# Performance work log

Measured on AMD Instinct MI355X. Metric: run time of the kernel, lower is better.

## Reference

```python
import jax, jax.numpy as jnp
import numpy as np

D_MODEL = 512
D_K = 64
D_V = 128
H = D_MODEL // D_V  # 4 heads (num_head = d_model // d_v per the source)
B, N = 4, 2048


def setup_inputs() -> dict:
    key = jax.random.key(0)
    k0, k1, k2, k3, k4 = jax.random.split(key, 5)
    s = 0.02
    return {
        "input_x": jax.random.normal(k0, (B, N, D_MODEL), jnp.float32),
        "Wq": jax.random.normal(k1, (D_MODEL, H * D_K), jnp.float32) * s,
        "Wk": jax.random.normal(k2, (D_MODEL, H * D_K), jnp.float32) * s,
        "Wv": jax.random.normal(k3, (D_MODEL, D_MODEL), jnp.float32) * s,
        "Wo": jax.random.normal(k4, (D_MODEL, D_MODEL), jnp.float32) * s,
    }


def reference(input_x, Wq, Wk, Wv, Wo):
    b, n, _ = input_x.shape
    # Contiguous per-head slices in the source == a simple reshape here.
    q = (input_x @ Wq).reshape(b, n, H, D_K)   # [B,N,H,dk]
    k = (input_x @ Wk).reshape(b, n, H, D_K)   # [B,N,H,dk]
    v = (input_x @ Wv).reshape(b, n, H, D_V)   # [B,N,H,dv]
    scale = jnp.sqrt(jnp.float32(D_K))
    scores = jnp.einsum('bqhd,bkhd->bhqk', q, k) / scale  # [B,H,N,N]
    # FAITHFUL quirk: the source uses nn.Softmax() with no dim on a 3D
    # (B,N,N) tensor; PyTorch's legacy dim inference picks dim=0 (batch).
    attn = jax.nn.softmax(scores, axis=0)
    out = jnp.einsum('bhqk,bkhd->bqhd', attn, v).reshape(b, n, H * D_V)
    return out @ Wo
```

## Files before the change

### kernel.cpp

```cpp
#include <hip/hip_runtime.h>
#include <hip/hip_bf16.h>


typedef __attribute__((ext_vector_type(8))) short short8;
typedef __attribute__((ext_vector_type(4))) float floatx4;
typedef unsigned short u16;
typedef unsigned int u32;

#define MFMA16(a, b, c) __builtin_amdgcn_mfma_f32_16x16x32_bf16((a), (b), (c), 0, 0, 0)

__device__ __forceinline__ u16 f2bf(float f) {
    union { float f; unsigned u; } v; v.f = f;
    unsigned r = v.u + 0x7fffu + ((v.u >> 16) & 1u);
    return (u16)(r >> 16);
}

__device__ __forceinline__ float bf2f(u16 b) {
    union { unsigned u; float f; } v; v.u = ((u32)b) << 16;
    return v.f;
}

__device__ __forceinline__ u32 pk2bf(float a, float b) {
#if __has_builtin(__builtin_amdgcn_cvt_pk_bf16_f32)
    typedef __attribute__((ext_vector_type(2))) __bf16 bf16x2;
    union { bf16x2 v; u32 u; } c;
    c.v = __builtin_amdgcn_cvt_pk_bf16_f32(a, b);
    return c.u;
#else
    return (u32)f2bf(a) | ((u32)f2bf(b) << 16);
#endif
}

__device__ __forceinline__ float ex2(float x) {
#if __has_builtin(__builtin_amdgcn_exp2f)
    return __builtin_amdgcn_exp2f(x);
#else
    return exp2f(x);
#endif
}

__device__ __forceinline__ void gload_lds16(const u16* g, u16* l) {
    __builtin_amdgcn_global_load_lds(
        (const __attribute__((address_space(1))) void*)(const void*)g,
        (__attribute__((address_space(3))) void*)(void*)l, 16, 0, 0);
}

__global__ __launch_bounds__(256) void prep_all_kernel(
    const float* __restrict__ x, u16* __restrict__ xb,
    const float* __restrict__ Wq, const float* __restrict__ Wk,
    const float* __restrict__ Wv, const float* __restrict__ Wo,
    u16* __restrict__ WallT, u16* __restrict__ WoT) {
    int bid = blockIdx.x;
    if (bid < 4096) {
        int i = bid * 256 + threadIdx.x;
        float4 v = ((const float4*)x)[i];
        ushort4 o;
        o.x = f2bf(v.x); o.y = f2bf(v.y); o.z = f2bf(v.z); o.w = f2bf(v.w);
        ((ushort4*)xb)[i] = o;
        return;
    }
    int i = (bid - 4096) * 256 + threadIdx.x;
    if (i < 524288) {
        int n = i >> 9, k = i & 511;
        float v;
        if (n < 256)      v = Wq[k * 256 + n] * 0.18033688011f;
        else if (n < 512) v = Wk[k * 256 + (n - 256)];
        else              v = Wv[k * 512 + (n - 512)];
        WallT[i] = f2bf(v);
    } else {
        int j = i - 524288;
        int n = j >> 9, k = j & 511;
        WoT[j] = f2bf(Wo[k * 512 + n]);
    }
}

__global__ __launch_bounds__(512) void gemm_qkv_kernel(
    const u16* __restrict__ A, const u16* __restrict__ BT,
    u16* __restrict__ Qp, u16* __restrict__ Kp, u16* __restrict__ Vp,
    int Kdim) {
    __shared__ u16 sm[16896];
    u16* Asl = sm;
    u16* Bsl = sm + 8192;
    const int tid = threadIdx.x;
    const int mbase = blockIdx.y * 128;
    const int nbase = blockIdx.x * 128;
    const int wave = tid >> 6, lane = tid & 63;
    const int wm = wave >> 2, wn = wave & 3;
    const int lq = lane & 15, quad = lane >> 4;

    const u16* gA = A + (size_t)(mbase + wave * 16 + (lane >> 3)) * Kdim + (lane & 7) * 8;
    const u16* gB = BT + (size_t)(nbase + wave * 16 + (lane >> 3)) * Kdim + (lane & 7) * 8;
    u16* lA = &Asl[(wave * 16) * 64];
    u16* lB = &Bsl[(wave * 16) * 64];

    const floatx4 z4 = {0.f, 0.f, 0.f, 0.f};
    floatx4 acc[4][2];
#pragma unroll
    for (int i = 0; i < 4; i++)
#pragma unroll
        for (int j = 0; j < 2; j++) acc[i][j] = z4;

    const int nk = Kdim >> 6;
    for (int kk = 0; kk < nk; kk++) {
        const int kb = kk << 6;
        if (kk) __syncthreads();
#pragma unroll
        for (int i = 0; i < 2; i++) {
            gload_lds16(gA + kb + (size_t)(i * 8) * Kdim, lA + (i * 8) * 64);
            gload_lds16(gB + kb + (size_t)(i * 8) * Kdim, lB + (i * 8) * 64);
        }
        __syncthreads();
#pragma unroll
        for (int ki = 0; ki < 2; ki++) {
            short8 af[4], bf[2];
#pragma unroll
            for (int mi = 0; mi < 4; mi++)
                af[mi] = *(const short8*)&Asl[(wm * 64 + mi * 16 + lq) * 64 + ki * 32 + quad * 8];
#pragma unroll
            for (int ni = 0; ni < 2; ni++)
                bf[ni] = *(const short8*)&Bsl[(wn * 32 + ni * 16 + lq) * 64 + ki * 32 + quad * 8];
#pragma unroll
            for (int mi = 0; mi < 4; mi++)
#pragma unroll
                for (int ni = 0; ni < 2; ni++)
                    acc[mi][ni] = MFMA16(af[mi], bf[ni], acc[mi][ni]);
        }
    }
    __syncthreads();
    const bool vtile = (nbase >= 512);
#pragma unroll
    for (int mi = 0; mi < 4; mi++)
#pragma unroll
        for (int ni = 0; ni < 2; ni++) {
            int cl = wn * 32 + ni * 16 + lq;
#pragma unroll
            for (int r = 0; r < 4; r++) {
                int rl = wm * 64 + mi * 16 + quad * 4 + r;
                if (vtile) sm[cl * 132 + rl] = f2bf(acc[mi][ni][r]);
                else       sm[rl * 132 + cl] = f2bf(acc[mi][ni][r]);
            }
        }
    __syncthreads();
    const int b = mbase >> 11;
    const int keyb = mbase & 2047;
    if (nbase < 256) {
        const int hq = nbase >> 6;
        const int qs_base = keyb >> 4;
#pragma unroll
        for (int t = 0; t < 4; t++) {
            int l = wave * 4 + t;
            int qs2 = l >> 2, h2 = (l >> 1) & 1, ki = l & 1;
            int qd = lane >> 4, lqq = lane & 15;
            short8 v = *(const short8*)&sm[(qs2 * 16 + lqq) * 132 + h2 * 64 + ki * 32 + qd * 8];
            int h = hq + h2;
            size_t base = ((size_t)(((b * 4 + h) * 128 + (qs_base + qs2)) * 2 + ki) * 64 + lane) << 3;
            *(short8*)&Qp[base] = v;
        }
    } else if (nbase < 512) {
        const int hb = (nbase - 256) >> 6;
        const int ktb = keyb >> 6;
#pragma unroll
        for (int t = 0; t < 4; t++) {
            int l = wave * 4 + t;
            int kt2 = l >> 4, hf = (l >> 3) & 1, nj = (l >> 2) & 1;
            int h2 = (l >> 1) & 1, ki = l & 1;
            int quadk = lane >> 4, lqk = lane & 15;
            short8 v = *(const short8*)&sm[(kt2 * 64 + hf * 32 + lqk * 2 + nj) * 132 +
                                           h2 * 64 + ki * 32 + quadk * 8];
            int h = hb + h2;
            size_t base = ((size_t)(((((b * 4 + h) * 32 + (ktb + kt2)) * 2 + hf) * 2 + nj)
                                    * 2 + ki) * 64 + lane) << 3;
            *(short8*)&Kp[base] = v;
        }
    } else {
        const int h = (nbase - 512) >> 7;
        const int ktb = keyb >> 6;
#pragma unroll
        for (int t = 0; t < 4; t++) {
            int l = wave * 4 + t;
            int kt2 = l >> 4, hf = (l >> 3) & 1, niv = (l >> 1) & 3, wv = l & 1;
            int quadv = lane >> 4, lqv = lane & 15;
            short8 v = *(const short8*)&sm[(hf * 64 + niv * 16 + lqv) * 132 +
                                           kt2 * 64 + wv * 32 + quadv * 8];
            size_t base = ((size_t)(((((b * 4 + h) * 32 + (ktb + kt2)) * 2 + hf) * 4 + niv)
                                    * 2 + wv) * 64 + lane) << 3;
            *(short8*)&Vp[base] = v;
        }
    }
}

__global__ __launch_bounds__(512) void gemm_out_kernel(
    const u16* __restrict__ A, const u16* __restrict__ BT,
    float* __restrict__ Cf, int Kdim, int ldc) {
    __shared__ u16 Asl[64 * 64];
    __shared__ u16 Bsl[128 * 64];
    const int tid = threadIdx.x;
    const int mbase = blockIdx.y * 64;
    const int nbase = blockIdx.x * 128;
    const int wave = tid >> 6, lane = tid & 63;
    const int wm = wave >> 2, wn = wave & 3;
    const int lq = lane & 15, quad = lane >> 4;

    const u16* gA = A + (size_t)(mbase + wave * 8 + (lane >> 3)) * Kdim + (lane & 7) * 8;
    const u16* gB = BT + (size_t)(nbase + wave * 16 + (lane >> 3)) * Kdim + (lane & 7) * 8;
    u16* lA = &Asl[(wave * 8) * 64];
    u16* lB = &Bsl[(wave * 16) * 64];

    const floatx4 z4 = {0.f, 0.f, 0.f, 0.f};
    floatx4 acc[2][2];
#pragma unroll
    for (int i = 0; i < 2; i++)
#pragma unroll
        for (int j = 0; j < 2; j++) acc[i][j] = z4;

    const int nk = Kdim >> 6;
    for (int kk = 0; kk < nk; kk++) {
        const int kb = kk << 6;
        if (kk) __syncthreads();
        gload_lds16(gA + kb, lA);
        gload_lds16(gB + kb, lB);
        gload_lds16(gB + kb + (size_t)8 * Kdim, lB + 8 * 64);
        __syncthreads();
#pragma unroll
        for (int ki = 0; ki < 2; ki++) {
            short8 af[2], bf[2];
#pragma unroll
            for (int mi = 0; mi < 2; mi++)
                af[mi] = *(const short8*)&Asl[(wm * 32 + mi * 16 + lq) * 64 + ki * 32 + quad * 8];
#pragma unroll
            for (int ni = 0; ni < 2; ni++)
                bf[ni] = *(const short8*)&Bsl[(wn * 32 + ni * 16 + lq) * 64 + ki * 32 + quad * 8];
#pragma unroll
            for (int mi = 0; mi < 2; mi++)
#pragma unroll
                for (int ni = 0; ni < 2; ni++)
                    acc[mi][ni] = MFMA16(af[mi], bf[ni], acc[mi][ni]);
        }
    }
#pragma unroll
    for (int mi = 0; mi < 2; mi++)
#pragma unroll
        for (int ni = 0; ni < 2; ni++)
#pragma unroll
            for (int r = 0; r < 4; r++)
                Cf[(size_t)(mbase + wm * 32 + mi * 16 + quad * 4 + r) * ldc +
                   (nbase + wn * 32 + ni * 16 + lq)] = acc[mi][ni][r];
}

__global__ __launch_bounds__(512) void attn_kernel(const u16* __restrict__ Qp,
                                                   const u16* __restrict__ Kp,
                                                   const u16* __restrict__ Vp,
                                                   u16* __restrict__ Pp) {
    __shared__ u16 pl[2 * 4 * 4096];
    const int bx = blockIdx.x;
    const int h = bx & 3;
    const int ck = (bx >> 2) & 3;
    const int qt = bx >> 4;
    const int tid = threadIdx.x;
    const int wave = tid >> 6, lane = tid & 63;
    const int mi = wave & 3, half = wave >> 2;
    const int dq = wave;
    const int half_v = dq >> 2, ni_v = dq & 3;
    const int lq = lane & 15, quad = lane >> 4;
    const int qs = qt * 4 + mi;

    short8 aq[4][2];
#pragma unroll
    for (int b = 0; b < 4; b++)
#pragma unroll
        for (int ki = 0; ki < 2; ki++)
            aq[b][ki] = *(const short8*)&Qp[
                ((size_t)((((b * 4 + h) * 128 + qs) * 2 + ki) * 64 + lane) << 3)];

    const floatx4 z4 = {0.f, 0.f, 0.f, 0.f};
    floatx4 oacc[4][4];
#pragma unroll
    for (int b = 0; b < 4; b++)
#pragma unroll
        for (int m2 = 0; m2 < 4; m2++) oacc[b][m2] = z4;

    for (int kt = ck * 8; kt < ck * 8 + 8; kt++) {
        u16* plb = &pl[((kt & 1) * 4 + mi) * 4096];
        u16* plbuf = &pl[(kt & 1) * 4 * 4096];
        floatx4 s[4][2];
#pragma unroll
        for (int b = 0; b < 4; b++) {
            const u16* kb = Kp +
                ((size_t)((((b * 4 + h) * 32 + kt) * 2 + half) * 2) << 10) +
                lane * 8;
#pragma unroll
            for (int nj = 0; nj < 2; nj++) {
                s[b][nj] = z4;
#pragma unroll
                for (int ki = 0; ki < 2; ki++)
                    s[b][nj] = MFMA16(aq[b][ki],
                                      *(const short8*)(kb + (nj * 2 + ki) * 512),
                                      s[b][nj]);
            }
        }
        short8 vf[4][2];
#pragma unroll
        for (int b = 0; b < 4; b++) {
            const u16* vb = Vp +
                ((size_t)(((((b * 4 + h) * 32 + kt) * 2 + half_v) * 4 + ni_v) * 2) << 9) +
                lane * 8;
            vf[b][0] = *(const short8*)vb;
            vf[b][1] = *(const short8*)(vb + 512);
        }
#pragma unroll
        for (int r = 0; r < 4; r++) {
            float e0a = ex2(s[0][0][r]), e0b = ex2(s[0][1][r]);
            float e1a = ex2(s[1][0][r]), e1b = ex2(s[1][1][r]);
            float e2a = ex2(s[2][0][r]), e2b = ex2(s[2][1][r]);
            float e3a = ex2(s[3][0][r]), e3b = ex2(s[3][1][r]);
            float ia = __builtin_amdgcn_rcpf(e0a + e1a + e2a + e3a);
            float ib = __builtin_amdgcn_rcpf(e0b + e1b + e2b + e3b);
            int q = quad * 4 + r;
            int col = (half * 32 + 2 * lq) ^ ((q & 7) * 8);
            *(u32*)&plb[(0 * 16 + q) * 64 + col] = pk2bf(e0a * ia, e0b * ib);
            *(u32*)&plb[(1 * 16 + q) * 64 + col] = pk2bf(e1a * ia, e1b * ib);
            *(u32*)&plb[(2 * 16 + q) * 64 + col] = pk2bf(e2a * ia, e2b * ib);
            *(u32*)&plb[(3 * 16 + q) * 64 + col] = pk2bf(e3a * ia, e3b * ib);
        }
        __syncthreads();
        const int sw = (lq & 7) * 8;
#pragma unroll
        for (int b = 0; b < 4; b++) {
#pragma unroll
            for (int m2 = 0; m2 < 4; m2++) {
                const u16* pm = plbuf + m2 * 4096;
                short8 ap0 = *(const short8*)&pm[(b * 16 + lq) * 64 + ((quad * 8) ^ sw)];
                short8 ap1 = *(const short8*)&pm[(b * 16 + lq) * 64 + ((32 + quad * 8) ^ sw)];
                oacc[b][m2] = MFMA16(ap0, vf[b][0], oacc[b][m2]);
                oacc[b][m2] = MFMA16(ap1, vf[b][1], oacc[b][m2]);
            }
        }
    }
    u16* Pc = Pp + (size_t)ck * (8192 * 512);
#pragma unroll
    for (int b = 0; b < 4; b++)
#pragma unroll
        for (int m2 = 0; m2 < 4; m2++)
#pragma unroll
            for (int r = 0; r < 4; r++)
                Pc[(size_t)(b * 2048 + qt * 64 + m2 * 16 + quad * 4 + r) * 512 +
                   h * 128 + dq * 16 + lq] = f2bf(oacc[b][m2][r]);
}

__global__ __launch_bounds__(256) void reduce4_kernel(u16* __restrict__ P) {
    const size_t S = (size_t)8192 * 512;
    size_t i = ((size_t)blockIdx.x * 256 + threadIdx.x) * 8;
    short8 a = *(short8*)&P[i];
    short8 b = *(short8*)&P[i + S];
    short8 c = *(short8*)&P[i + 2 * S];
    short8 d = *(short8*)&P[i + 3 * S];
    short8 o;
#pragma unroll
    for (int j = 0; j < 8; j++) {
        float s = bf2f((u16)a[j]) + bf2f((u16)b[j]) +
                  bf2f((u16)c[j]) + bf2f((u16)d[j]);
        o[j] = (short)f2bf(s);
    }
    *(short8*)&P[i] = o;
}

extern "C" void kernel_launch(void* const* d_in, const int* in_sizes, int n_in,
                              void* d_out, int out_size, void* d_ws, size_t ws_size,
                              hipStream_t stream) {
    const float* x  = (const float*)d_in[0];
    const float* Wq = (const float*)d_in[1];
    const float* Wk = (const float*)d_in[2];
    const float* Wv = (const float*)d_in[3];
    const float* Wo = (const float*)d_in[4];
    float* out = (float*)d_out;

    char* ws = (char*)d_ws;
    u16* Pp    = (u16*)ws;
    u16* Xb    = (u16*)ws;
    u16* WallT = (u16*)(ws + (size_t)8 * 1024 * 1024);
    char* tail = ws + (size_t)32 * 1024 * 1024;
    u16* WoT   = (u16*)tail; tail += (size_t)512 * 512 * 2;
    u16* Qp    = (u16*)tail; tail += (size_t)8192 * 256 * 2;
    u16* Kp    = (u16*)tail; tail += (size_t)8192 * 256 * 2;
    u16* Vp    = (u16*)tail; tail += (size_t)8192 * 512 * 2;

    prep_all_kernel<<<7168, 256, 0, stream>>>(x, Xb, Wq, Wk, Wv, Wo, WallT, WoT);
    gemm_qkv_kernel<<<dim3(8, 64), 512, 0, stream>>>(Xb, WallT, Qp, Kp, Vp, 512);
    attn_kernel<<<512, 512, 0, stream>>>(Qp, Kp, Vp, Pp);
    reduce4_kernel<<<2048, 256, 0, stream>>>(Pp);
    gemm_out_kernel<<<dim3(4, 128), 512, 0, stream>>>(Pp, WoT, out, 512, 512);
}
```

Baseline: 166.2 us.

## Fuse split-K partial reduction into output GEMM, remap blocks per XCD, add setprio

Drops the separate reduce4 kernel. The output GEMM now sums the four split-K partial buffers while it loads its A tile, so it reads them directly instead of using async global-to-LDS copies for A. Block indices in all three kernels are remapped so that neighbouring tiles land on the same XCD, for better L2 locality. s_setprio is raised around the MFMA sections of the attention kernel. This saves one launch and a write/read round trip of P, at the cost of more A traffic (each A tile is reread by four N-blocks) and synchronous loads in the GEMM.

```diff
diff --git a/kernel.cpp b/kernel.cpp
--- a/kernel.cpp
+++ b/kernel.cpp
@@ -82,8 +82,10 @@
     u16* Asl = sm;
     u16* Bsl = sm + 8192;
     const int tid = threadIdx.x;
-    const int mbase = blockIdx.y * 128;
-    const int nbase = blockIdx.x * 128;
+    const int bid0 = blockIdx.y * 8 + blockIdx.x;
+    const int xcd = bid0 & 7, jj = bid0 >> 3;
+    const int mbase = (xcd * 8 + (jj >> 3)) * 128;
+    const int nbase = (jj & 7) * 128;
     const int wave = tid >> 6, lane = tid & 63;
     const int wm = wave >> 2, wn = wave & 3;
     const int lq = lane & 15, quad = lane >> 4;
@@ -195,15 +197,18 @@
     __shared__ u16 Asl[64 * 64];
     __shared__ u16 Bsl[128 * 64];
     const int tid = threadIdx.x;
-    const int mbase = blockIdx.y * 64;
-    const int nbase = blockIdx.x * 128;
+    const int bid0 = blockIdx.y * 4 + blockIdx.x;
+    const int xcd = bid0 & 7, jj = bid0 >> 3;
+    const int mbase = (xcd * 16 + (jj >> 2)) * 64;
+    const int nbase = (jj & 3) * 128;
     const int wave = tid >> 6, lane = tid & 63;
     const int wm = wave >> 2, wn = wave & 3;
     const int lq = lane & 15, quad = lane >> 4;
+    const size_t S = (size_t)8192 * 512;
 
     const u16* gA = A + (size_t)(mbase + wave * 8 + (lane >> 3)) * Kdim + (lane & 7) * 8;
     const u16* gB = BT + (size_t)(nbase + wave * 16 + (lane >> 3)) * Kdim + (lane & 7) * 8;
-    u16* lA = &Asl[(wave * 8) * 64];
+    u16* lAw = &Asl[(wave * 8 + (lane >> 3)) * 64 + (lane & 7) * 8];
     u16* lB = &Bsl[(wave * 16) * 64];
 
     const floatx4 z4 = {0.f, 0.f, 0.f, 0.f};
@@ -216,10 +221,21 @@
     const int nk = Kdim >> 6;
     for (int kk = 0; kk < nk; kk++) {
         const int kb = kk << 6;
+        short8 p0 = *(const short8*)(gA + kb);
+        short8 p1 = *(const short8*)(gA + kb + S);
+        short8 p2 = *(const short8*)(gA + kb + 2 * S);
+        short8 p3 = *(const short8*)(gA + kb + 3 * S);
         if (kk) __syncthreads();
-        gload_lds16(gA + kb, lA);
         gload_lds16(gB + kb, lB);
         gload_lds16(gB + kb + (size_t)8 * Kdim, lB + 8 * 64);
+        short8 o;
+#pragma unroll
+        for (int j2 = 0; j2 < 8; j2++) {
+            float s = bf2f((u16)p0[j2]) + bf2f((u16)p1[j2]) +
+                      bf2f((u16)p2[j2]) + bf2f((u16)p3[j2]);
+            o[j2] = (short)f2bf(s);
+        }
+        *(short8*)lAw = o;
         __syncthreads();
 #pragma unroll
         for (int ki = 0; ki < 2; ki++) {
@@ -253,9 +269,12 @@
                                                    u16* __restrict__ Pp) {
     __shared__ u16 pl[2 * 4 * 4096];
     const int bx = blockIdx.x;
-    const int h = bx & 3;
-    const int ck = (bx >> 2) & 3;
-    const int qt = bx >> 4;
+    const int xcd = bx & 7;
+    const int j8 = bx >> 3;
+    const int sl = xcd * 2 + (j8 >> 5);
+    const int h = sl & 3;
+    const int ck = sl >> 2;
+    const int qt = j8 & 31;
     const int tid = threadIdx.x;
     const int wave = tid >> 6, lane = tid & 63;
     const int mi = wave & 3, half = wave >> 2;
@@ -283,6 +302,7 @@
         u16* plb = &pl[((kt & 1) * 4 + mi) * 4096];
         u16* plbuf = &pl[(kt & 1) * 4 * 4096];
         floatx4 s[4][2];
+        __builtin_amdgcn_s_setprio(1);
 #pragma unroll
         for (int b = 0; b < 4; b++) {
             const u16* kb = Kp +
@@ -298,6 +318,7 @@
                                       s[b][nj]);
             }
         }
+        __builtin_amdgcn_s_setprio(0);
         short8 vf[4][2];
 #pragma unroll
         for (int b = 0; b < 4; b++) {
@@ -324,6 +345,7 @@
         }
         __syncthreads();
         const int sw = (lq & 7) * 8;
+        __builtin_amdgcn_s_setprio(1);
 #pragma unroll
         for (int b = 0; b < 4; b++) {
 #pragma unroll
@@ -335,6 +357,7 @@
                 oacc[b][m2] = MFMA16(ap1, vf[b][1], oacc[b][m2]);
             }
         }
+        __builtin_amdgcn_s_setprio(0);
     }
     u16* Pc = Pp + (size_t)ck * (8192 * 512);
 #pragma unroll
@@ -345,23 +368,6 @@
             for (int r = 0; r < 4; r++)
                 Pc[(size_t)(b * 2048 + qt * 64 + m2 * 16 + quad * 4 + r) * 512 +
                    h * 128 + dq * 16 + lq] = f2bf(oacc[b][m2][r]);
-}
-
-__global__ __launch_bounds__(256) void reduce4_kernel(u16* __restrict__ P) {
-    const size_t S = (size_t)8192 * 512;
-    size_t i = ((size_t)blockIdx.x * 256 + threadIdx.x) * 8;
-    short8 a = *(short8*)&P[i];
-    short8 b = *(short8*)&P[i + S];
-    short8 c = *(short8*)&P[i + 2 * S];
-    short8 d = *(short8*)&P[i + 3 * S];
-    short8 o;
-#pragma unroll
-    for (int j = 0; j < 8; j++) {
-        float s = bf2f((u16)a[j]) + bf2f((u16)b[j]) +
-                  bf2f((u16)c[j]) + bf2f((u16)d[j]);
-        o[j] = (short)f2bf(s);
-    }
-    *(short8*)&P[i] = o;
 }
 
 extern "C" void kernel_launch(void* const* d_in, const int* in_sizes, int n_in,
@@ -387,6 +393,5 @@
     prep_all_kernel<<<7168, 256, 0, stream>>>(x, Xb, Wq, Wk, Wv, Wo, WallT, WoT);
     gemm_qkv_kernel<<<dim3(8, 64), 512, 0, stream>>>(Xb, WallT, Qp, Kp, Vp, 512);
     attn_kernel<<<512, 512, 0, stream>>>(Qp, Kp, Vp, Pp);
-    reduce4_kernel<<<2048, 256, 0, stream>>>(Pp);
     gemm_out_kernel<<<dim3(4, 128), 512, 0, stream>>>(Pp, WoT, out, 512, 512);
 }
```

Result: no change. 165.5 us (-0.4%).
